# Kernel tuning notes

Measured on AMD Instinct MI355X. Metric: run time of the kernel, lower is better.

The kernel has to match this reference:

```python
import jax, jax.numpy as jnp
import numpy as np

N_NODES = 50000
N_EDGES = 800000
D_IN = 256
D_HID = 256
D_OUT = 256
BN_EPS = 1e-5
NORM_EPS = 1e-12


def _glorot(key, out_dim, in_dim):
    a = np.sqrt(6.0 / (in_dim + out_dim)).astype(np.float32)
    return jax.random.uniform(key, (out_dim, in_dim), jnp.float32, -a, a)


def setup_inputs() -> dict:
    key = jax.random.key(0)
    ks = jax.random.split(key, 8)
    x = jax.random.normal(ks[0], (N_NODES, D_IN), jnp.float32)
    edge_index = jax.random.randint(ks[1], (2, N_EDGES), 0, N_NODES, dtype=jnp.int32)
    batch = jnp.zeros((N_NODES,), jnp.int32)
    return {
        "x": x,
        "W1_l": _glorot(ks[2], D_HID, D_IN),
        "b1_l": jnp.zeros((D_HID,), jnp.float32),
        "W1_r": _glorot(ks[3], D_HID, D_IN),
        "W2_l": _glorot(ks[4], D_OUT, D_HID),
        "b2_l": jnp.zeros((D_OUT,), jnp.float32),
        "W2_r": _glorot(ks[5], D_OUT, D_HID),
        "gamma1": jnp.ones((D_HID,), jnp.float32),
        "beta1": jnp.zeros((D_HID,), jnp.float32),
        "edge_index": edge_index,
        "batch": batch,
    }


def _sage_conv(x, W_l, b_l, W_r, src, dst, n_nodes):
    # PyG SAGEConv (aggr='mean'): out = lin_l(mean_j x_j) + lin_r(x)
    msgs = x[src]                                            # [E, d] gather
    s = jax.ops.segment_sum(msgs, dst, num_segments=n_nodes)  # [N, d] scatter-add
    cnt = jax.ops.segment_sum(jnp.ones((src.shape[0], 1), x.dtype), dst,
                              num_segments=n_nodes)
    agg = jnp.where(cnt > 0, s / jnp.maximum(cnt, 1.0), 0.0)
    return agg @ W_l.T + b_l + x @ W_r.T


def _batch_norm(h, gamma, beta):
    mu = jnp.mean(h, axis=0)
    var = jnp.mean((h - mu) ** 2, axis=0)  # biased, as torch train-mode BN
    return (h - mu) * jax.lax.rsqrt(var + BN_EPS) * gamma + beta


def _l2_normalize(h):
    n = jnp.linalg.norm(h, axis=-1, keepdims=True)
    return h / jnp.maximum(n, NORM_EPS)


def reference(x, W1_l, b1_l, W1_r, W2_l, b2_l, W2_r, gamma1, beta1,
              edge_index, batch):
    n = x.shape[0]
    src, dst = edge_index[0], edge_index[1]
    # layer 1: SAGEConv -> BN (train stats) -> ReLU (dropout = identity in eval)
    h = _sage_conv(x, W1_l, b1_l, W1_r, src, dst, n)
    h = jax.nn.relu(_batch_norm(h, gamma1, beta1))
    # layer 2: SAGEConv -> L2 normalize
    h = _sage_conv(h, W2_l, b2_l, W2_r, src, dst, n)
    node_emb = _l2_normalize(h)
    # global mean pool over batch ids (single graph here), then normalize
    gsum = jax.ops.segment_sum(node_emb, batch, num_segments=1)
    gcnt = jax.ops.segment_sum(jnp.ones((n, 1), node_emb.dtype), batch,
                               num_segments=1)
    graph_emb = _l2_normalize(gsum / jnp.maximum(gcnt, 1.0))
    return node_emb, graph_emb
```

## Files before the change

### kernel.cpp

```cpp
#include <hip/hip_runtime.h>
#include <math.h>

#define NN 50000
#define NE 800000
#define D  256
#define SCB 196

typedef unsigned short u16;
typedef __attribute__((ext_vector_type(8))) short short8;
typedef __attribute__((ext_vector_type(8))) unsigned short u16x8;
typedef __attribute__((ext_vector_type(4))) float f32x4;

__device__ __forceinline__ u16 f2b(float f) {
    unsigned u = __float_as_uint(f);
    return (u16)((u + 0x7FFFu + ((u >> 16) & 1u)) >> 16);
}
__device__ __forceinline__ float b2f(u16 b) {
    return __uint_as_float(((unsigned)b) << 16);
}

__device__ __forceinline__ void gl16(const u16* g, u16* l) {
    __builtin_amdgcn_global_load_lds(
        (const __attribute__((address_space(1))) void*)g,
        (__attribute__((address_space(3))) void*)l, 16, 0, 0);
}

__global__ void wxconv_kernel(const float* __restrict__ x,
                              const float* __restrict__ W1l, const float* __restrict__ W1r,
                              const float* __restrict__ W2l, const float* __restrict__ W2r,
                              const int* __restrict__ dst,
                              u16* __restrict__ Acat,
                              u16* __restrict__ Wcat1, u16* __restrict__ Wcat2,
                              int* __restrict__ deg) {
    int b = blockIdx.x;
    if (b < 12500) {
        int idx = b * 256 + threadIdx.x;
        int r = idx >> 6;
        int c4 = (idx & 63) * 4;
        float4 v = *(const float4*)&x[(size_t)r * 256 + c4];
        ushort4 o;
        o.x = f2b(v.x); o.y = f2b(v.y); o.z = f2b(v.z); o.w = f2b(v.w);
        *(ushort4*)&Acat[(size_t)r * 512 + 256 + c4] = o;
    } else if (b < 12756) {
        int r = b - 12500;
        int j = threadIdx.x;
        Wcat1[r * 512 + j]       = f2b(W1l[r * 256 + j]);
        Wcat1[r * 512 + 256 + j] = f2b(W1r[r * 256 + j]);
        Wcat2[r * 512 + j]       = f2b(W2l[r * 256 + j]);
        Wcat2[r * 512 + 256 + j] = f2b(W2r[r * 256 + j]);
    } else {
        int e0 = ((b - 12756) * 256 + threadIdx.x) * 4;
        if (e0 + 3 < NE) {
            int4 d = *(const int4*)&dst[e0];
            atomicAdd(&deg[d.x], 1);
            atomicAdd(&deg[d.y], 1);
            atomicAdd(&deg[d.z], 1);
            atomicAdd(&deg[d.w], 1);
        } else {
            for (int e = e0; e < NE; e++) atomicAdd(&deg[dst[e]], 1);
        }
    }
}

__global__ void scanA_kernel(const int* __restrict__ deg, int* __restrict__ partial) {
    int t = threadIdx.x;
    int i = blockIdx.x * 256 + t;
    int v = (i < NN) ? deg[i] : 0;
#pragma unroll
    for (int o = 32; o; o >>= 1) v += __shfl_xor(v, o);
    __shared__ int sm[4];
    if ((t & 63) == 0) sm[t >> 6] = v;
    __syncthreads();
    if (t == 0) partial[blockIdx.x] = sm[0] + sm[1] + sm[2] + sm[3];
}

__global__ void scanB_kernel(const int* __restrict__ partial, int* __restrict__ base,
                             int* __restrict__ offs) {
    __shared__ int sm[256];
    int t = threadIdx.x;
    int v = (t < SCB) ? partial[t] : 0;
    sm[t] = v;
    __syncthreads();
    for (int off = 1; off < 256; off <<= 1) {
        int u = 0;
        if (t >= off) u = sm[t - off];
        __syncthreads();
        sm[t] += u;
        __syncthreads();
    }
    if (t < SCB) base[t] = sm[t] - v;
    if (t == 255) offs[NN] = sm[255];
}

__global__ void scanC_kernel(const int* __restrict__ deg, const int* __restrict__ base,
                             int* __restrict__ offs, int* __restrict__ cur) {
    __shared__ int sm[256];
    int t = threadIdx.x;
    int i = blockIdx.x * 256 + t;
    int v = (i < NN) ? deg[i] : 0;
    sm[t] = v;
    __syncthreads();
    for (int off = 1; off < 256; off <<= 1) {
        int u = 0;
        if (t >= off) u = sm[t - off];
        __syncthreads();
        sm[t] += u;
        __syncthreads();
    }
    int o = base[blockIdx.x] + sm[t] - v;
    if (i < NN) {
        offs[i] = o;
        cur[i] = o;
    }
}

__global__ void fill_kernel(const int* __restrict__ src, const int* __restrict__ dst,
                            int* __restrict__ cur, int* __restrict__ csr) {
    int e0 = (blockIdx.x * blockDim.x + threadIdx.x) * 8;
    if (e0 + 7 < NE) {
        int4 d0 = *(const int4*)&dst[e0];
        int4 d1 = *(const int4*)&dst[e0 + 4];
        int4 s0 = *(const int4*)&src[e0];
        int4 s1 = *(const int4*)&src[e0 + 4];
        int p0 = atomicAdd(&cur[d0.x], 1);
        int p1 = atomicAdd(&cur[d0.y], 1);
        int p2 = atomicAdd(&cur[d0.z], 1);
        int p3 = atomicAdd(&cur[d0.w], 1);
        int p4 = atomicAdd(&cur[d1.x], 1);
        int p5 = atomicAdd(&cur[d1.y], 1);
        int p6 = atomicAdd(&cur[d1.z], 1);
        int p7 = atomicAdd(&cur[d1.w], 1);
        csr[p0] = s0.x; csr[p1] = s0.y; csr[p2] = s0.z; csr[p3] = s0.w;
        csr[p4] = s1.x; csr[p5] = s1.y; csr[p6] = s1.z; csr[p7] = s1.w;
    } else {
        for (int e = e0; e < NE; e++) {
            int pos = atomicAdd(&cur[dst[e]], 1);
            csr[pos] = src[e];
        }
    }
}

__global__ __launch_bounds__(256)
void agg_kernel(const u16* __restrict__ Acat, const int* __restrict__ csr,
                const int* __restrict__ offs, u16* __restrict__ AcatW) {
    int wid = (blockIdx.x * blockDim.x + threadIdx.x) >> 6;
    int lane = threadIdx.x & 63;
    if (wid >= NN) return;
    int beg = offs[wid];
    int end = offs[wid + 1];
    int deg = end - beg;
    int half = lane >> 5;
    int lc = (lane & 31) * 8;
    int mid = beg + ((deg + 1) >> 1);
    int e  = half ? mid : beg;
    int hi = half ? end : mid;
    float a[8] = {0.f, 0.f, 0.f, 0.f, 0.f, 0.f, 0.f, 0.f};
    for (; e + 7 < hi; e += 8) {
        int s0 = csr[e + 0], s1 = csr[e + 1], s2 = csr[e + 2], s3 = csr[e + 3];
        int s4 = csr[e + 4], s5 = csr[e + 5], s6 = csr[e + 6], s7 = csr[e + 7];
        u16x8 v0 = *(const u16x8*)&Acat[(size_t)s0 * 512 + 256 + lc];
        u16x8 v1 = *(const u16x8*)&Acat[(size_t)s1 * 512 + 256 + lc];
        u16x8 v2 = *(const u16x8*)&Acat[(size_t)s2 * 512 + 256 + lc];
        u16x8 v3 = *(const u16x8*)&Acat[(size_t)s3 * 512 + 256 + lc];
        u16x8 v4 = *(const u16x8*)&Acat[(size_t)s4 * 512 + 256 + lc];
        u16x8 v5 = *(const u16x8*)&Acat[(size_t)s5 * 512 + 256 + lc];
        u16x8 v6 = *(const u16x8*)&Acat[(size_t)s6 * 512 + 256 + lc];
        u16x8 v7 = *(const u16x8*)&Acat[(size_t)s7 * 512 + 256 + lc];
#pragma unroll
        for (int i = 0; i < 8; i++)
            a[i] += ((b2f(v0[i]) + b2f(v1[i])) + (b2f(v2[i]) + b2f(v3[i]))) +
                    ((b2f(v4[i]) + b2f(v5[i])) + (b2f(v6[i]) + b2f(v7[i])));
    }
    for (; e + 3 < hi; e += 4) {
        int s0 = csr[e + 0], s1 = csr[e + 1], s2 = csr[e + 2], s3 = csr[e + 3];
        u16x8 v0 = *(const u16x8*)&Acat[(size_t)s0 * 512 + 256 + lc];
        u16x8 v1 = *(const u16x8*)&Acat[(size_t)s1 * 512 + 256 + lc];
        u16x8 v2 = *(const u16x8*)&Acat[(size_t)s2 * 512 + 256 + lc];
        u16x8 v3 = *(const u16x8*)&Acat[(size_t)s3 * 512 + 256 + lc];
#pragma unroll
        for (int i = 0; i < 8; i++)
            a[i] += (b2f(v0[i]) + b2f(v1[i])) + (b2f(v2[i]) + b2f(v3[i]));
    }
    for (; e < hi; e++) {
        int s0 = csr[e];
        u16x8 v0 = *(const u16x8*)&Acat[(size_t)s0 * 512 + 256 + lc];
#pragma unroll
        for (int i = 0; i < 8; i++) a[i] += b2f(v0[i]);
    }
#pragma unroll
    for (int i = 0; i < 8; i++) a[i] += __shfl_xor(a[i], 32);
    float sc = (deg > 0) ? 1.0f / (float)deg : 0.0f;
    if (half == 0) {
        u16x8 o;
#pragma unroll
        for (int i = 0; i < 8; i++) o[i] = f2b(a[i] * sc);
        *(u16x8*)&AcatW[(size_t)wid * 512 + lc] = o;
    }
}

template<int BF16_OUT>
__global__ __launch_bounds__(256)
void mfma_gemm_kernel(const u16* __restrict__ A, const u16* __restrict__ W,
                      const float* __restrict__ bias, void* __restrict__ Cout) {
    __shared__ u16 As[4][128 * 32];
    __shared__ u16 Bs[4][128 * 32];
    const int tid = threadIdx.x;
    const int l = tid & 63;
    const int wid = tid >> 6;
    const int wr = wid >> 1, wc = wid & 1;
    const int row0 = blockIdx.x * 128;
    const int col0 = blockIdx.y * 128;

    const u16* aptr[2];
    const u16* bptr[2];
#pragma unroll
    for (int i = 0; i < 2; i++) {
        int row = wid * 32 + i * 16 + (l >> 2);
        int kg = (l & 3) ^ ((row >> 1) & 3);
        int ra = row0 + row;
        if (ra > NN - 1) ra = NN - 1;
        aptr[i] = A + (size_t)ra * 512 + kg * 8;
        bptr[i] = W + (size_t)(col0 + row) * 512 + kg * 8;
    }

    f32x4 acc[4][4] = {};

#define STAGE(b, t)                                                          \
    do {                                                                     \
        _Pragma("unroll") for (int i_ = 0; i_ < 2; i_++) {                   \
            u16* al = &As[b][(wid * 32 + i_ * 16) * 32];                     \
            u16* bl = &Bs[b][(wid * 32 + i_ * 16) * 32];                     \
            gl16(aptr[i_] + (t) * 32, al);                                   \
            gl16(bptr[i_] + (t) * 32, bl);                                   \
        }                                                                    \
    } while (0)

    STAGE(0, 0);
    STAGE(1, 1);

    const int kq = l >> 4;
    const int sw = ((l & 15) >> 1) & 3;
#pragma unroll
    for (int t = 0; t < 16; t++) {
        if (t + 2 < 16) STAGE((t + 2) & 3, t + 2);

        if (t < 14)       asm volatile("s_waitcnt vmcnt(8)" ::: "memory");
        else if (t == 14) asm volatile("s_waitcnt vmcnt(4)" ::: "memory");
        else              asm volatile("s_waitcnt vmcnt(0)" ::: "memory");
        __builtin_amdgcn_s_barrier();
        __builtin_amdgcn_sched_barrier(0);

        short8 af[4], bf[4];
#pragma unroll
        for (int m = 0; m < 4; m++) {
            int row = wr * 64 + m * 16 + (l & 15);
            af[m] = *(const short8*)&As[t & 3][row * 32 + (kq ^ sw) * 8];
        }
#pragma unroll
        for (int n = 0; n < 4; n++) {
            int row = wc * 64 + n * 16 + (l & 15);
            bf[n] = *(const short8*)&Bs[t & 3][row * 32 + (kq ^ sw) * 8];
        }
#pragma unroll
        for (int m = 0; m < 4; m++)
#pragma unroll
            for (int n = 0; n < 4; n++)
                acc[m][n] = __builtin_amdgcn_mfma_f32_16x16x32_bf16(
                    af[m], bf[n], acc[m][n], 0, 0, 0);
    }
#undef STAGE

    const int cq = l >> 4;
    const int cc = l & 15;
#pragma unroll
    for (int m = 0; m < 4; m++) {
#pragma unroll
        for (int n = 0; n < 4; n++) {
            int c = col0 + wc * 64 + n * 16 + cc;
#pragma unroll
            for (int j = 0; j < 4; j++) {
                int r = row0 + wr * 64 + m * 16 + cq * 4 + j;
                if (r < NN) {
                    float v = acc[m][n][j] + bias[c];
                    if (BF16_OUT)
                        ((u16*)Cout)[(size_t)r * 256 + c] = f2b(v);
                    else
                        ((float*)Cout)[(size_t)r * 256 + c] = v;
                }
            }
        }
    }
}

__global__ void colstats_kernel(const u16* __restrict__ h, float* __restrict__ stats) {
    int j = threadIdx.x;
    float s0 = 0.f, s1 = 0.f;
    for (int r = blockIdx.x; r < NN; r += gridDim.x) {
        float v = b2f(h[(size_t)r * 256 + j]);
        s0 += v;
        s1 += v * v;
    }
    atomicAdd(&stats[j], s0);
    atomicAdd(&stats[256 + j], s1);
}

__global__ void bnrelu_kernel(const u16* __restrict__ hb,
                              const float* __restrict__ stats,
                              const float* __restrict__ gamma,
                              const float* __restrict__ beta,
                              u16* __restrict__ Acat) {
    __shared__ float s_scale[256], s_shift[256];
    int t = threadIdx.x;
    {
        const float invN = 1.0f / (float)NN;
        float mu = stats[t] * invN;
        float var = stats[256 + t] * invN - mu * mu;
        float sc = gamma[t] * rsqrtf(var + 1e-5f);
        s_scale[t] = sc;
        s_shift[t] = beta[t] - mu * sc;
    }
    __syncthreads();
    int idx = blockIdx.x * 256 + t;
    int r = idx >> 5;
    int c8 = (idx & 31) * 8;
    u16x8 v = *(const u16x8*)&hb[(size_t)r * 256 + c8];
    u16x8 o;
#pragma unroll
    for (int i = 0; i < 8; i++) {
        float f = b2f(v[i]) * s_scale[c8 + i] + s_shift[c8 + i];
        o[i] = f2b(fmaxf(f, 0.f));
    }
    *(u16x8*)&Acat[(size_t)r * 512 + 256 + c8] = o;
}

__global__ __launch_bounds__(512)
void l2norm_kernel(float* __restrict__ out, float* __restrict__ gsum) {
    __shared__ float sm[8 * 256];
    int wave = threadIdx.x >> 6;
    int lane = threadIdx.x & 63;
    float c0 = 0.f, c1 = 0.f, c2 = 0.f, c3 = 0.f;
    for (int r = blockIdx.x * 8 + wave; r < NN; r += gridDim.x * 8) {
        float4 v = *(float4*)&out[(size_t)r * 256 + lane * 4];
        float sq = v.x * v.x + v.y * v.y + v.z * v.z + v.w * v.w;
#pragma unroll
        for (int o = 32; o; o >>= 1) sq += __shfl_xor(sq, o);
        float invn = 1.0f / fmaxf(sqrtf(sq), 1e-12f);
        v.x *= invn; v.y *= invn; v.z *= invn; v.w *= invn;
        *(float4*)&out[(size_t)r * 256 + lane * 4] = v;
        c0 += v.x; c1 += v.y; c2 += v.z; c3 += v.w;
    }
    *(float4*)&sm[wave * 256 + lane * 4] = make_float4(c0, c1, c2, c3);
    __syncthreads();
    int t = threadIdx.x;
    if (t < 256) {
        float s = 0.f;
#pragma unroll
        for (int w = 0; w < 8; w++) s += sm[w * 256 + t];
        atomicAdd(&gsum[t], s);
    }
}

__global__ void graph_kernel(const float* __restrict__ gsum, float* __restrict__ gout) {
    __shared__ float wsum[4];
    int j = threadIdx.x;
    float v = gsum[j] * (1.0f / (float)NN);
    float sq = v * v;
#pragma unroll
    for (int o = 32; o; o >>= 1) sq += __shfl_xor(sq, o);
    if ((j & 63) == 0) wsum[j >> 6] = sq;
    __syncthreads();
    float tot = wsum[0] + wsum[1] + wsum[2] + wsum[3];
    gout[j] = v / fmaxf(sqrtf(tot), 1e-12f);
}

extern "C" void kernel_launch(void* const* d_in, const int* in_sizes, int n_in,
                              void* d_out, int out_size, void* d_ws, size_t ws_size,
                              hipStream_t stream) {
    const float* x      = (const float*)d_in[0];
    const float* W1_l   = (const float*)d_in[1];
    const float* b1_l   = (const float*)d_in[2];
    const float* W1_r   = (const float*)d_in[3];
    const float* W2_l   = (const float*)d_in[4];
    const float* b2_l   = (const float*)d_in[5];
    const float* W2_r   = (const float*)d_in[6];
    const float* gamma1 = (const float*)d_in[7];
    const float* beta1  = (const float*)d_in[8];
    const int*   eidx   = (const int*)d_in[9];
    const int* src = eidx;
    const int* dst = eidx + NE;

    char* wsb = (char*)d_ws;
    int*   deg   = (int*)(wsb + 0);
    int*   offs  = (int*)(wsb + 200000);
    int*   cur   = (int*)(wsb + 400004);
    int*   csr   = (int*)(wsb + 600004);
    int*   part  = (int*)(wsb + 3800064);
    int*   base  = (int*)(wsb + 3801088);
    float* stats = (float*)(wsb + 3802112);
    float* gsum  = (float*)(wsb + 3804160);
    u16*   Wcat1 = (u16*)(wsb + 3807232);
    u16*   Wcat2 = (u16*)(wsb + 4069376);
    u16*   hb    = (u16*)(wsb + 4331520);
    u16*   Acat  = (u16*)(wsb + 29931520);
    float* out   = (float*)d_out;
    float* gout  = out + (size_t)NN * 256;

    hipMemsetAsync(deg, 0, NN * sizeof(int), stream);
    hipMemsetAsync(stats, 0, 3072, stream);

    const int DEGB = (NE / 4 + 255) / 256;
    wxconv_kernel<<<12756 + DEGB, 256, 0, stream>>>(x, W1_l, W1_r, W2_l, W2_r,
                                                    dst, Acat, Wcat1, Wcat2, deg);

    scanA_kernel<<<SCB, 256, 0, stream>>>(deg, part);
    scanB_kernel<<<1, 256, 0, stream>>>(part, base, offs);
    scanC_kernel<<<SCB, 256, 0, stream>>>(deg, base, offs, cur);
    fill_kernel<<<(NE / 8 + 255) / 256, 256, 0, stream>>>(src, dst, cur, csr);

    dim3 ggrid((NN + 127) / 128, 2);

    agg_kernel<<<12500, 256, 0, stream>>>(Acat, csr, offs, Acat);
    mfma_gemm_kernel<1><<<ggrid, 256, 0, stream>>>(Acat, Wcat1, b1_l, hb);
    colstats_kernel<<<512, 256, 0, stream>>>(hb, stats);
    bnrelu_kernel<<<6250, 256, 0, stream>>>(hb, stats, gamma1, beta1, Acat);

    agg_kernel<<<12500, 256, 0, stream>>>(Acat, csr, offs, Acat);
    mfma_gemm_kernel<0><<<ggrid, 256, 0, stream>>>(Acat, Wcat2, b2_l, out);

    l2norm_kernel<<<1024, 512, 0, stream>>>(out, gsum);
    graph_kernel<<<1, 256, 0, stream>>>(gsum, gout);
}
```

Measured before the change: 387.4 us.

## Fuse layer-2 GEMM with row L2 normalization and per-block column sums

The second GEMM now computes a full 256-column row tile per block (128x256) with a 3-stage LDS pipeline, so each block can compute row norms in-register, normalize, and write the final fp32 output once. Per-block column partial sums replace the atomics in the old separate l2norm kernel, and graph_kernel reduces those partials. This removes a full read/write pass over the 50000x256 fp32 output and a kernel launch, at the cost of a larger accumulator footprint and only 391 blocks, which may lower occupancy and parallelism. The partial sums reuse the CSR workspace region, which is dead by that point.

```diff
diff --git a/kernel.cpp b/kernel.cpp
--- a/kernel.cpp
+++ b/kernel.cpp
@@ -5,6 +5,7 @@
 #define NE 800000
 #define D  256
 #define SCB 196
+#define NB2 391
 
 typedef unsigned short u16;
 typedef __attribute__((ext_vector_type(8))) short short8;
@@ -198,10 +199,9 @@
     }
 }
 
-template<int BF16_OUT>
 __global__ __launch_bounds__(256)
 void mfma_gemm_kernel(const u16* __restrict__ A, const u16* __restrict__ W,
-                      const float* __restrict__ bias, void* __restrict__ Cout) {
+                      const float* __restrict__ bias, u16* __restrict__ Cout) {
     __shared__ u16 As[4][128 * 32];
     __shared__ u16 Bs[4][128 * 32];
     const int tid = threadIdx.x;
@@ -225,24 +225,22 @@
 
     f32x4 acc[4][4] = {};
 
-#define STAGE(b, t)                                                          \
+#define STAGE1(b, t)                                                         \
     do {                                                                     \
         _Pragma("unroll") for (int i_ = 0; i_ < 2; i_++) {                   \
-            u16* al = &As[b][(wid * 32 + i_ * 16) * 32];                     \
-            u16* bl = &Bs[b][(wid * 32 + i_ * 16) * 32];                     \
-            gl16(aptr[i_] + (t) * 32, al);                                   \
-            gl16(bptr[i_] + (t) * 32, bl);                                   \
+            gl16(aptr[i_] + (t) * 32, &As[b][(wid * 32 + i_ * 16) * 32]);    \
+            gl16(bptr[i_] + (t) * 32, &Bs[b][(wid * 32 + i_ * 16) * 32]);    \
         }                                                                    \
     } while (0)
 
-    STAGE(0, 0);
-    STAGE(1, 1);
+    STAGE1(0, 0);
+    STAGE1(1, 1);
 
     const int kq = l >> 4;
     const int sw = ((l & 15) >> 1) & 3;
 #pragma unroll
     for (int t = 0; t < 16; t++) {
-        if (t + 2 < 16) STAGE((t + 2) & 3, t + 2);
+        if (t + 2 < 16) STAGE1((t + 2) & 3, t + 2);
 
         if (t < 14)       asm volatile("s_waitcnt vmcnt(8)" ::: "memory");
         else if (t == 14) asm volatile("s_waitcnt vmcnt(4)" ::: "memory");
@@ -268,7 +266,7 @@
                 acc[m][n] = __builtin_amdgcn_mfma_f32_16x16x32_bf16(
                     af[m], bf[n], acc[m][n], 0, 0, 0);
     }
-#undef STAGE
+#undef STAGE1
 
     const int cq = l >> 4;
     const int cc = l & 15;
@@ -280,16 +278,152 @@
 #pragma unroll
             for (int j = 0; j < 4; j++) {
                 int r = row0 + wr * 64 + m * 16 + cq * 4 + j;
-                if (r < NN) {
-                    float v = acc[m][n][j] + bias[c];
-                    if (BF16_OUT)
-                        ((u16*)Cout)[(size_t)r * 256 + c] = f2b(v);
-                    else
-                        ((float*)Cout)[(size_t)r * 256 + c] = v;
+                if (r < NN)
+                    Cout[(size_t)r * 256 + c] = f2b(acc[m][n][j] + bias[c]);
+            }
+        }
+    }
+}
+
+__global__ __launch_bounds__(256)
+void gemm2_l2_kernel(const u16* __restrict__ A, const u16* __restrict__ W,
+                     const float* __restrict__ bias, float* __restrict__ out,
+                     float* __restrict__ colsum_part) {
+    __shared__ u16 As[3][128 * 32];
+    __shared__ u16 Bs[3][256 * 32];
+    const int tid = threadIdx.x;
+    const int l = tid & 63;
+    const int wid = tid >> 6;
+    const int wr = wid >> 1, wc = wid & 1;
+    const int row0 = blockIdx.x * 128;
+
+    const u16* aptr[2];
+    const u16* bptr[4];
+#pragma unroll
+    for (int i = 0; i < 2; i++) {
+        int row = wid * 32 + i * 16 + (l >> 2);
+        int kg = (l & 3) ^ ((row >> 1) & 3);
+        int ra = row0 + row;
+        if (ra > NN - 1) ra = NN - 1;
+        aptr[i] = A + (size_t)ra * 512 + kg * 8;
+    }
+#pragma unroll
+    for (int i = 0; i < 4; i++) {
+        int row = wid * 64 + i * 16 + (l >> 2);
+        int kg = (l & 3) ^ ((row >> 1) & 3);
+        bptr[i] = W + (size_t)row * 512 + kg * 8;
+    }
+
+    f32x4 acc[4][8] = {};
+
+#define STAGE2(b, t)                                                         \
+    do {                                                                     \
+        _Pragma("unroll") for (int i_ = 0; i_ < 2; i_++)                     \
+            gl16(aptr[i_] + (t) * 32, &As[b][(wid * 32 + i_ * 16) * 32]);    \
+        _Pragma("unroll") for (int i_ = 0; i_ < 4; i_++)                     \
+            gl16(bptr[i_] + (t) * 32, &Bs[b][(wid * 64 + i_ * 16) * 32]);    \
+    } while (0)
+
+    STAGE2(0, 0);
+    STAGE2(1, 1);
+
+    const int kq = l >> 4;
+    const int sw = ((l & 15) >> 1) & 3;
+#pragma unroll
+    for (int t = 0; t < 16; t++) {
+        if (t < 15) asm volatile("s_waitcnt vmcnt(6)" ::: "memory");
+        else        asm volatile("s_waitcnt vmcnt(0)" ::: "memory");
+        __builtin_amdgcn_s_barrier();
+        __builtin_amdgcn_sched_barrier(0);
+
+        if (t + 2 < 16) STAGE2((t + 2) % 3, t + 2);
+
+        short8 af[4], bf[8];
+#pragma unroll
+        for (int m = 0; m < 4; m++) {
+            int row = wr * 64 + m * 16 + (l & 15);
+            af[m] = *(const short8*)&As[t % 3][row * 32 + (kq ^ sw) * 8];
+        }
+#pragma unroll
+        for (int n = 0; n < 8; n++) {
+            int row = wc * 128 + n * 16 + (l & 15);
+            bf[n] = *(const short8*)&Bs[t % 3][row * 32 + (kq ^ sw) * 8];
+        }
+#pragma unroll
+        for (int m = 0; m < 4; m++)
+#pragma unroll
+            for (int n = 0; n < 8; n++)
+                acc[m][n] = __builtin_amdgcn_mfma_f32_16x16x32_bf16(
+                    af[m], bf[n], acc[m][n], 0, 0, 0);
+    }
+#undef STAGE2
+
+    float* rowsq = (float*)&As[1][0];
+    float* colp  = rowsq + 256;
+    const int cq = l >> 4;
+    const int cc = l & 15;
+
+    float sq[4][4];
+#pragma unroll
+    for (int m = 0; m < 4; m++)
+#pragma unroll
+        for (int j = 0; j < 4; j++) {
+            float s = 0.f;
+#pragma unroll
+            for (int n = 0; n < 8; n++) {
+                float v = acc[m][n][j] + bias[wc * 128 + n * 16 + cc];
+                acc[m][n][j] = v;
+                s += v * v;
+            }
+            sq[m][j] = s;
+        }
+#pragma unroll
+    for (int o = 1; o < 16; o <<= 1)
+#pragma unroll
+        for (int m = 0; m < 4; m++)
+#pragma unroll
+            for (int j = 0; j < 4; j++) sq[m][j] += __shfl_xor(sq[m][j], o);
+
+    __syncthreads();
+#pragma unroll
+    for (int m = 0; m < 4; m++)
+#pragma unroll
+        for (int j = 0; j < 4; j++)
+            if (cc == j) rowsq[wc * 128 + wr * 64 + m * 16 + cq * 4 + j] = sq[m][j];
+    __syncthreads();
+
+    float colpart[8] = {0.f, 0.f, 0.f, 0.f, 0.f, 0.f, 0.f, 0.f};
+#pragma unroll
+    for (int m = 0; m < 4; m++)
+#pragma unroll
+        for (int j = 0; j < 4; j++) {
+            int rl = wr * 64 + m * 16 + cq * 4 + j;
+            float s = rowsq[rl] + rowsq[128 + rl];
+            float invn = 1.0f / fmaxf(sqrtf(s), 1e-12f);
+            int r = row0 + rl;
+            bool ok = (r < NN);
+#pragma unroll
+            for (int n = 0; n < 8; n++) {
+                float vn = acc[m][n][j] * invn;
+                if (ok) {
+                    out[(size_t)r * 256 + wc * 128 + n * 16 + cc] = vn;
+                    colpart[n] += vn;
                 }
             }
         }
-    }
+#pragma unroll
+    for (int n = 0; n < 8; n++) {
+        colpart[n] += __shfl_xor(colpart[n], 16);
+        colpart[n] += __shfl_xor(colpart[n], 32);
+    }
+    if (l < 16) {
+#pragma unroll
+        for (int n = 0; n < 8; n++)
+            colp[wr * 256 + wc * 128 + n * 16 + l] = colpart[n];
+    }
+    __syncthreads();
+    if (tid < 256)
+        colsum_part[(size_t)blockIdx.x * 256 + tid] = colp[tid] + colp[256 + tid];
 }
 
 __global__ void colstats_kernel(const u16* __restrict__ h, float* __restrict__ stats) {
@@ -333,37 +467,14 @@
     *(u16x8*)&Acat[(size_t)r * 512 + 256 + c8] = o;
 }
 
-__global__ __launch_bounds__(512)
-void l2norm_kernel(float* __restrict__ out, float* __restrict__ gsum) {
-    __shared__ float sm[8 * 256];
-    int wave = threadIdx.x >> 6;
-    int lane = threadIdx.x & 63;
-    float c0 = 0.f, c1 = 0.f, c2 = 0.f, c3 = 0.f;
-    for (int r = blockIdx.x * 8 + wave; r < NN; r += gridDim.x * 8) {
-        float4 v = *(float4*)&out[(size_t)r * 256 + lane * 4];
-        float sq = v.x * v.x + v.y * v.y + v.z * v.z + v.w * v.w;
-#pragma unroll
-        for (int o = 32; o; o >>= 1) sq += __shfl_xor(sq, o);
-        float invn = 1.0f / fmaxf(sqrtf(sq), 1e-12f);
-        v.x *= invn; v.y *= invn; v.z *= invn; v.w *= invn;
-        *(float4*)&out[(size_t)r * 256 + lane * 4] = v;
-        c0 += v.x; c1 += v.y; c2 += v.z; c3 += v.w;
-    }
-    *(float4*)&sm[wave * 256 + lane * 4] = make_float4(c0, c1, c2, c3);
-    __syncthreads();
-    int t = threadIdx.x;
-    if (t < 256) {
-        float s = 0.f;
-#pragma unroll
-        for (int w = 0; w < 8; w++) s += sm[w * 256 + t];
-        atomicAdd(&gsum[t], s);
-    }
-}
-
-__global__ void graph_kernel(const float* __restrict__ gsum, float* __restrict__ gout) {
+__global__ void graph_kernel(const float* __restrict__ colsum_part,
+                             float* __restrict__ gout) {
     __shared__ float wsum[4];
     int j = threadIdx.x;
-    float v = gsum[j] * (1.0f / (float)NN);
+    float s = 0.f;
+#pragma unroll 8
+    for (int b = 0; b < NB2; b++) s += colsum_part[(size_t)b * 256 + j];
+    float v = s * (1.0f / (float)NN);
     float sq = v * v;
 #pragma unroll
     for (int o = 32; o; o >>= 1) sq += __shfl_xor(sq, o);
@@ -390,23 +501,23 @@
     const int* dst = eidx + NE;
 
     char* wsb = (char*)d_ws;
-    int*   deg   = (int*)(wsb + 0);
-    int*   offs  = (int*)(wsb + 200000);
-    int*   cur   = (int*)(wsb + 400004);
-    int*   csr   = (int*)(wsb + 600004);
-    int*   part  = (int*)(wsb + 3800064);
-    int*   base  = (int*)(wsb + 3801088);
-    float* stats = (float*)(wsb + 3802112);
-    float* gsum  = (float*)(wsb + 3804160);
-    u16*   Wcat1 = (u16*)(wsb + 3807232);
-    u16*   Wcat2 = (u16*)(wsb + 4069376);
-    u16*   hb    = (u16*)(wsb + 4331520);
-    u16*   Acat  = (u16*)(wsb + 29931520);
-    float* out   = (float*)d_out;
-    float* gout  = out + (size_t)NN * 256;
+    int*   deg    = (int*)(wsb + 0);
+    int*   offs   = (int*)(wsb + 200000);
+    int*   cur    = (int*)(wsb + 400004);
+    int*   csr    = (int*)(wsb + 600004);
+    float* cspart = (float*)(wsb + 600004);
+    int*   part   = (int*)(wsb + 3800064);
+    int*   base   = (int*)(wsb + 3801088);
+    float* stats  = (float*)(wsb + 3802112);
+    u16*   Wcat1  = (u16*)(wsb + 3807232);
+    u16*   Wcat2  = (u16*)(wsb + 4069376);
+    u16*   hb     = (u16*)(wsb + 4331520);
+    u16*   Acat   = (u16*)(wsb + 29931520);
+    float* out    = (float*)d_out;
+    float* gout   = out + (size_t)NN * 256;
 
     hipMemsetAsync(deg, 0, NN * sizeof(int), stream);
-    hipMemsetAsync(stats, 0, 3072, stream);
+    hipMemsetAsync(stats, 0, 2048, stream);
 
     const int DEGB = (NE / 4 + 255) / 256;
     wxconv_kernel<<<12756 + DEGB, 256, 0, stream>>>(x, W1_l, W1_r, W2_l, W2_r,
@@ -417,16 +528,15 @@
     scanC_kernel<<<SCB, 256, 0, stream>>>(deg, base, offs, cur);
     fill_kernel<<<(NE / 8 + 255) / 256, 256, 0, stream>>>(src, dst, cur, csr);
 
-    dim3 ggrid((NN + 127) / 128, 2);
+    dim3 ggrid(NB2, 2);
 
     agg_kernel<<<12500, 256, 0, stream>>>(Acat, csr, offs, Acat);
-    mfma_gemm_kernel<1><<<ggrid, 256, 0, stream>>>(Acat, Wcat1, b1_l, hb);
+    mfma_gemm_kernel<<<ggrid, 256, 0, stream>>>(Acat, Wcat1, b1_l, hb);
     colstats_kernel<<<512, 256, 0, stream>>>(hb, stats);
     bnrelu_kernel<<<6250, 256, 0, stream>>>(hb, stats, gamma1, beta1, Acat);
 
     agg_kernel<<<12500, 256, 0, stream>>>(Acat, csr, offs, Acat);
-    mfma_gemm_kernel<0><<<ggrid, 256, 0, stream>>>(Acat, Wcat2, b2_l, out);
-
-    l2norm_kernel<<<1024, 512, 0, stream>>>(out, gsum);
-    graph_kernel<<<1, 256, 0, stream>>>(gsum, gout);
-}
+    gemm2_l2_kernel<<<NB2, 256, 0, stream>>>(Acat, Wcat2, b2_l, out, cspart);
+
+    graph_kernel<<<1, 256, 0, stream>>>(cspart, gout);
+}
```

After: 382.0 us. About the same (-1.4%).
